# Kernel tuning notes

Hardware: AMD Instinct MI355X
Metric: run time of the kernel (lower is better)

## Reference

```python
import jax, jax.numpy as jnp
import numpy as np

B, T, C, H = 4, 2048, 1024, 16
D = C // H


def setup_inputs() -> dict:
    key = jax.random.key(0)
    ks = jax.random.split(key, 5)
    s = 0.02
    return {
        "x": jax.random.normal(ks[0], (B, T, C), dtype=jnp.float32),
        "W_attn": jax.random.normal(ks[1], (C, 3 * C), dtype=jnp.float32) * s,
        "b_attn": jax.random.normal(ks[2], (3 * C,), dtype=jnp.float32) * s,
        "W_proj": jax.random.normal(ks[3], (C, C), dtype=jnp.float32) * s,
        "b_proj": jax.random.normal(ks[4], (C,), dtype=jnp.float32) * s,
    }


def reference(x, W_attn, b_attn, W_proj, b_proj):
    # QKV projection: [B,T,3C]
    qkv = x @ W_attn + b_attn
    q, k, v = jnp.split(qkv, 3, axis=-1)
    # [B,T,C] -> [B,H,T,D]
    def to_heads(t):
        return t.reshape(B, T, H, D).transpose(0, 2, 1, 3)
    q, k, v = to_heads(q), to_heads(k), to_heads(v)
    scale = 1.0 / np.sqrt(D).astype(np.float32)
    # full (non-causal) attention scores [B,H,T,T]
    att = jnp.einsum("bhqd,bhkd->bhqk", q, k) * scale
    att = jax.nn.softmax(att, axis=-1)
    y = jnp.einsum("bhqk,bhkd->bhqd", att, v)
    y = y.transpose(0, 2, 1, 3).reshape(B, T, C)
    return y @ W_proj + b_proj
```

## Files before the change

### kernel.cpp

```cpp
#include <hip/hip_runtime.h>

#define BATCH 4
#define SEQ   2048
#define CDIM  1024
#define NHEAD 16
#define HDIM  64
#define BH    (BATCH * NHEAD)
#define MROWS (BATCH * SEQ)

typedef __attribute__((ext_vector_type(8))) short  short8;
typedef __attribute__((ext_vector_type(4))) float  floatx4;

#define MFMA_BF16(a, b, c) __builtin_amdgcn_mfma_f32_16x16x32_bf16((a), (b), (c), 0, 0, 0)

#define GLOAD16(g, l) __builtin_amdgcn_global_load_lds( \
    (__attribute__((address_space(1))) void*)(g),       \
    (__attribute__((address_space(3))) void*)(l), 16, 0, 0)

__device__ __forceinline__ unsigned short f2bf(float f) {
    union { float f; unsigned u; } v; v.f = f;
    unsigned u = v.u;
    return (unsigned short)((u + 0x7FFFu + ((u >> 16) & 1u)) >> 16);
}

__device__ __forceinline__ float fast_exp2(float x) {
#if __has_builtin(__builtin_amdgcn_exp2f)
    return __builtin_amdgcn_exp2f(x);
#else
    return exp2f(x);
#endif
}

__device__ __forceinline__ unsigned pack_bf16_trunc(float a, float b) {
    union { float f; unsigned u; } ua, ub;
    ua.f = a; ub.f = b;
    return __builtin_amdgcn_perm(ub.u, ua.u, 0x07060302u);
}

__global__ __launch_bounds__(256) void conv_bf16_kernel(
    const float* __restrict__ in, unsigned short* __restrict__ out)
{
    int i = (blockIdx.x * 256 + threadIdx.x) * 4;
    float4 v = *(const float4*)(in + i);
    ushort4 o;
    o.x = f2bf(v.x); o.y = f2bf(v.y); o.z = f2bf(v.z); o.w = f2bf(v.w);
    *(ushort4*)(out + i) = o;
}

__global__ __launch_bounds__(256) void conv_wt_kernel(
    const float* __restrict__ in, unsigned short* __restrict__ out, int K, int N)
{
    __shared__ float T[64][68];
    const int k0 = blockIdx.y * 64, n0 = blockIdx.x * 64;
    const int tid = threadIdx.x;
    const int r = tid >> 4, c4 = (tid & 15) * 4;
    #pragma unroll
    for (int i = 0; i < 4; ++i) {
        int row = r + i * 16;
        float4 v = *(const float4*)(in + (size_t)(k0 + row) * N + n0 + c4);
        T[row][c4 + 0] = v.x; T[row][c4 + 1] = v.y;
        T[row][c4 + 2] = v.z; T[row][c4 + 3] = v.w;
    }
    __syncthreads();
    #pragma unroll
    for (int i = 0; i < 4; ++i) {
        int nrow = r + i * 16;
        ushort4 o;
        o.x = f2bf(T[c4 + 0][nrow]); o.y = f2bf(T[c4 + 1][nrow]);
        o.z = f2bf(T[c4 + 2][nrow]); o.w = f2bf(T[c4 + 3][nrow]);
        *(ushort4*)(out + (size_t)(n0 + nrow) * K + k0 + c4) = o;
    }
}

__global__ __launch_bounds__(512, 2) void qkv_mfma_kernel(
    const unsigned short* __restrict__ A,
    const unsigned short* __restrict__ Bt,
    const float* __restrict__ bias,
    unsigned short* __restrict__ Qo,
    unsigned short* __restrict__ Ko,
    unsigned short* __restrict__ Vo)
{
    __shared__ __align__(16) unsigned short L[2 * 32768];

    const int tid = threadIdx.x;
    const int m0 = blockIdx.y * 256, n0 = blockIdx.x * 256;
    const int w = tid >> 6, lane = tid & 63;
    const int wr = w >> 2, wc = w & 3;
    const int lm = lane & 15, kg = lane >> 4;
    const int sw = lm & 7;

    floatx4 acc[2][4][2][2];
    const floatx4 zf = {0.f, 0.f, 0.f, 0.f};
    #pragma unroll
    for (int a = 0; a < 2; ++a)
        #pragma unroll
        for (int b = 0; b < 4; ++b)
            #pragma unroll
            for (int c = 0; c < 2; ++c)
                #pragma unroll
                for (int d = 0; d < 2; ++d) acc[a][b][c][d] = zf;

    short8 af[4][2], bf[2][2];

#define QSTAGE_A(B_, H_, KT_) do {                                            \
    unsigned short* _l = (unsigned short*)L + (B_) * 32768 + (H_) * 8192;     \
    _Pragma("unroll")                                                         \
    for (int _i = 0; _i < 2; ++_i) {                                          \
        int _s = _i * 512 + tid, _r = _s >> 3, _c = _s & 7;                   \
        GLOAD16(A + (size_t)(m0 + (H_) * 128 + _r) * CDIM + (KT_) * 64        \
                   + ((_c ^ (_r & 7)) * 8), _l + _s * 8);                     \
    } } while (0)

#define QSTAGE_B(B_, H_, KT_) do {                                            \
    unsigned short* _l = (unsigned short*)L + (B_) * 32768 + 16384 + (H_) * 8192; \
    _Pragma("unroll")                                                         \
    for (int _i = 0; _i < 2; ++_i) {                                          \
        int _s = _i * 512 + tid, _r = _s >> 3, _c = _s & 7;                   \
        GLOAD16(Bt + (size_t)(n0 + (H_) * 128 + _r) * CDIM + (KT_) * 64       \
                   + ((_c ^ (_r & 7)) * 8), _l + _s * 8);                     \
    } } while (0)

#define QLOAD_A(B_, H_) do {                                                  \
    const unsigned short* _p = (const unsigned short*)L + (B_) * 32768 + (H_) * 8192; \
    _Pragma("unroll")                                                         \
    for (int _m = 0; _m < 4; ++_m) {                                          \
        int _row = wr * 64 + _m * 16 + lm;                                    \
        _Pragma("unroll")                                                     \
        for (int _k = 0; _k < 2; ++_k)                                        \
            af[_m][_k] = *(const short8*)(_p + _row * 64                      \
                          + (((_k * 4 + kg) ^ sw) * 8));                      \
    } } while (0)

#define QLOAD_B(B_, H_) do {                                                  \
    const unsigned short* _p = (const unsigned short*)L + (B_) * 32768 + 16384 + (H_) * 8192; \
    _Pragma("unroll")                                                         \
    for (int _n = 0; _n < 2; ++_n) {                                          \
        int _row = wc * 32 + _n * 16 + lm;                                    \
        _Pragma("unroll")                                                     \
        for (int _k = 0; _k < 2; ++_k)                                        \
            bf[_n][_k] = *(const short8*)(_p + _row * 64                      \
                          + (((_k * 4 + kg) ^ sw) * 8));                      \
    } } while (0)

#define QMFMA(HH_, HP_) do {                                                  \
    _Pragma("unroll") for (int _k = 0; _k < 2; ++_k)                          \
    _Pragma("unroll") for (int _m = 0; _m < 4; ++_m)                          \
    _Pragma("unroll") for (int _n = 0; _n < 2; ++_n)                          \
        acc[HH_][_m][HP_][_n] =                                               \
            MFMA_BF16(af[_m][_k], bf[_n][_k], acc[HH_][_m][HP_][_n]);         \
    } while (0)

#define QPHASE(HH_, HP_, LA_, LB_, STAGE_, VM_) do {                          \
    if (LA_) QLOAD_A(buf, HH_);                                               \
    if (LB_) QLOAD_B(buf, HP_);                                               \
    STAGE_;                                                                   \
    asm volatile("s_waitcnt vmcnt(" #VM_ ")" ::: "memory");                   \
    __builtin_amdgcn_s_barrier();                                             \
    asm volatile("s_waitcnt lgkmcnt(0)" ::: "memory");                        \
    __builtin_amdgcn_sched_barrier(0);                                        \
    __builtin_amdgcn_s_setprio(1);                                            \
    QMFMA(HH_, HP_);                                                          \
    __builtin_amdgcn_s_setprio(0);                                            \
    __builtin_amdgcn_s_barrier();                                             \
    __builtin_amdgcn_sched_barrier(0);                                        \
    } while (0)

    QSTAGE_A(0, 0, 0); QSTAGE_B(0, 0, 0); QSTAGE_B(0, 1, 0); QSTAGE_A(0, 1, 0);
    asm volatile("s_waitcnt vmcnt(4)" ::: "memory");
    __builtin_amdgcn_s_barrier();

    #pragma unroll 1
    for (int t = 0; t < CDIM / 64 - 1; ++t) {
        const int buf = t & 1, nb = buf ^ 1;
        QPHASE(0, 0, 1, 1, QSTAGE_A(nb, 0, t + 1), 4);
        QPHASE(0, 1, 0, 1, QSTAGE_B(nb, 0, t + 1), 4);
        QPHASE(1, 1, 1, 0, QSTAGE_B(nb, 1, t + 1), 4);
        QPHASE(1, 0, 0, 1, QSTAGE_A(nb, 1, t + 1), 4);
    }
    {
        const int buf = (CDIM / 64 - 1) & 1;
        QPHASE(0, 0, 1, 1, ((void)0), 2);
        QPHASE(0, 1, 0, 1, ((void)0), 0);
        QPHASE(1, 1, 1, 0, ((void)0), 0);
        QPHASE(1, 0, 0, 1, ((void)0), 0);
    }

#undef QPHASE
#undef QMFMA
#undef QLOAD_B
#undef QLOAD_A
#undef QSTAGE_B
#undef QSTAGE_A

    #pragma unroll
    for (int hp = 0; hp < 2; ++hp) {
        #pragma unroll
        for (int nt = 0; nt < 2; ++nt) {
            int col = n0 + hp * 128 + wc * 32 + nt * 16 + lm;
            float bv = bias[col];
            int which = col >> 10;
            int c1 = col & 1023;
            int h = c1 >> 6, d = c1 & 63;
            #pragma unroll
            for (int hh = 0; hh < 2; ++hh) {
                #pragma unroll
                for (int mt = 0; mt < 4; ++mt) {
                    int m = m0 + hh * 128 + wr * 64 + mt * 16 + kg * 4;
                    int b = m >> 11;
                    int tt = m & 2047;
                    int bh = b * NHEAD + h;
                    floatx4 a = acc[hh][mt][hp][nt];
                    if (which == 2) {
                        ushort4 o;
                        o.x = f2bf(a[0] + bv);
                        o.y = f2bf(a[1] + bv);
                        o.z = f2bf(a[2] + bv);
                        o.w = f2bf(a[3] + bv);
                        *(ushort4*)(Vo + ((size_t)bh * 64 + d) * SEQ + tt) = o;
                    } else {
                        unsigned short* dst = (which == 0) ? Qo : Ko;
                        float qs = (which == 0) ? 0.18033688011112042f : 1.0f;
                        #pragma unroll
                        for (int r = 0; r < 4; ++r)
                            dst[((size_t)bh * SEQ + tt + r) * 64 + d] =
                                f2bf((a[r] + bv) * qs);
                    }
                }
            }
        }
    }
}

#define GBUF (128 * 32)

__device__ __forceinline__ void gemm_stage(
    const unsigned short* __restrict__ A, const unsigned short* __restrict__ Bt,
    int K, int m0, int n0, int k0, unsigned short* As, unsigned short* Bs, int tid)
{
    #pragma unroll
    for (int i = 0; i < 2; ++i) {
        int ci = i * 256 + tid;
        GLOAD16(A  + (size_t)(m0 + (ci >> 2)) * K + k0 + (ci & 3) * 8, As + ci * 8);
        GLOAD16(Bt + (size_t)(n0 + (ci >> 2)) * K + k0 + (ci & 3) * 8, Bs + ci * 8);
    }
}

__global__ __launch_bounds__(256) void proj_mfma_kernel(
    const unsigned short* __restrict__ A,
    const unsigned short* __restrict__ Bt,
    const float* __restrict__ bias,
    float* __restrict__ out)
{
    const int K = CDIM;
    __shared__ __align__(16) unsigned short As2[2 * GBUF];
    __shared__ __align__(16) unsigned short Bs2[2 * GBUF];

    const int tid = threadIdx.x;
    const int m0 = blockIdx.y * 128, n0 = blockIdx.x * 128;
    const int w = tid >> 6, lane = tid & 63;
    const int wm = (w >> 1) * 64, wn = (w & 1) * 64;
    const int lm = lane & 15, kg = lane >> 4;

    floatx4 acc[4][4];
    const floatx4 zf = {0.f, 0.f, 0.f, 0.f};
    #pragma unroll
    for (int mt = 0; mt < 4; ++mt)
        #pragma unroll
        for (int nt = 0; nt < 4; ++nt) acc[mt][nt] = zf;

    gemm_stage(A, Bt, K, m0, n0, 0, As2, Bs2, tid);

    #pragma unroll 1
    for (int kt = 0; kt < K / 32; ++kt) {
        __syncthreads();
        if (kt + 1 < K / 32)
            gemm_stage(A, Bt, K, m0, n0, (kt + 1) * 32,
                       As2 + ((kt + 1) & 1) * GBUF, Bs2 + ((kt + 1) & 1) * GBUF, tid);
        const unsigned short* As = As2 + (kt & 1) * GBUF;
        const unsigned short* Bs = Bs2 + (kt & 1) * GBUF;
        short8 af[4], bfr[4];
        #pragma unroll
        for (int t = 0; t < 4; ++t) {
            af[t]  = *(const short8*)(As + (wm + t * 16 + lm) * 32 + kg * 8);
            bfr[t] = *(const short8*)(Bs + (wn + t * 16 + lm) * 32 + kg * 8);
        }
        #pragma unroll
        for (int mt = 0; mt < 4; ++mt)
            #pragma unroll
            for (int nt = 0; nt < 4; ++nt)
                acc[mt][nt] = MFMA_BF16(af[mt], bfr[nt], acc[mt][nt]);
    }

    #pragma unroll
    for (int nt = 0; nt < 4; ++nt) {
        int col = n0 + wn + nt * 16 + lm;
        float bv = bias[col];
        #pragma unroll
        for (int mt = 0; mt < 4; ++mt) {
            int mbase = m0 + wm + mt * 16 + kg * 4;
            #pragma unroll
            for (int r = 0; r < 4; ++r)
                out[(size_t)(mbase + r) * CDIM + col] = acc[mt][nt][r] + bv;
        }
    }
}

#define BUFSH 8192

__device__ __forceinline__ void attn_stage_tile(
    const unsigned short* __restrict__ Kg,
    const unsigned short* __restrict__ Vg,
    size_t base, int kb, unsigned short* buf, int tid)
{
    unsigned short* Kb_ = buf;
    unsigned short* Vb_ = buf + 4096;
    #pragma unroll
    for (int i = 0; i < 2; ++i) {
        int lin = i * 256 + tid;
        int srow = lin >> 3;
        int chunk = lin & 7;
        int s2 = srow & 31;
        int grow = (srow & 32) + ((s2 >> 2) & 3) * 8 + ((s2 >> 4) & 1) * 4 + (s2 & 3);
        int gch = chunk ^ (srow & 7);
        GLOAD16(Kg + base + (size_t)(kb * 64 + grow) * 64 + gch * 8, Kb_ + lin * 8);
        GLOAD16(Vg + base + (size_t)srow * SEQ + kb * 64 + gch * 8, Vb_ + lin * 8);
    }
}

__global__ __launch_bounds__(256) void attn_mfma_kernel(
    const unsigned short* __restrict__ Qg,
    const unsigned short* __restrict__ Kg,
    const unsigned short* __restrict__ Vg,
    unsigned short* __restrict__ Y)
{
    __shared__ __align__(16) unsigned short Smem[2 * BUFSH];

    const int tid = threadIdx.x, w = tid >> 6, lane = tid & 63;
    const int lm = lane & 15, kg = lane >> 4;
    const int qb = blockIdx.x, bh = blockIdx.y;
    const size_t base = (size_t)bh * SEQ * 64;

    short8 qf[2][2];
    #pragma unroll
    for (int nt = 0; nt < 2; ++nt)
        #pragma unroll
        for (int c = 0; c < 2; ++c)
            qf[nt][c] = *(const short8*)(
                Qg + base + (size_t)(qb * 128 + w * 32 + nt * 16 + lm) * 64 + c * 32 + kg * 8);

    const floatx4 zf = {0.f, 0.f, 0.f, 0.f};
    floatx4 O[2][4];
    #pragma unroll
    for (int nt = 0; nt < 2; ++nt)
        #pragma unroll
        for (int nd = 0; nd < 4; ++nd) O[nt][nd] = zf;
    float lsum[2] = {0.f, 0.f};

    attn_stage_tile(Kg, Vg, base, 0, Smem, tid);

    #pragma unroll 1
    for (int kb = 0; kb < SEQ / 64; ++kb) {
        __syncthreads();
        if (kb + 1 < SEQ / 64)
            attn_stage_tile(Kg, Vg, base, kb + 1, Smem + ((kb + 1) & 1) * BUFSH, tid);

        const unsigned short* Ksb = Smem + (kb & 1) * BUFSH;
        const unsigned short* Vsb = Ksb + 4096;
        const int sw = (lm & 7);

        #pragma unroll
        for (int ch = 0; ch < 2; ++ch) {
            uint4 pa[2];
            #pragma unroll
            for (int mt = 0; mt < 2; ++mt) {
                floatx4 st[2];
                #pragma unroll
                for (int nt = 0; nt < 2; ++nt) st[nt] = zf;
                #pragma unroll
                for (int c = 0; c < 2; ++c) {
                    short8 kf = *(const short8*)(
                        Ksb + (ch * 32 + mt * 16 + lm) * 64 + ((c * 4 + kg) ^ sw) * 8);
                    #pragma unroll
                    for (int nt = 0; nt < 2; ++nt)
                        st[nt] = MFMA_BF16(kf, qf[nt][c], st[nt]);
                }
                #pragma unroll
                for (int nt = 0; nt < 2; ++nt) {
                    float e0 = fast_exp2(st[nt][0]);
                    float e1 = fast_exp2(st[nt][1]);
                    float e2 = fast_exp2(st[nt][2]);
                    float e3 = fast_exp2(st[nt][3]);
                    lsum[nt] += (e0 + e1) + (e2 + e3);
                    if (mt == 0) {
                        pa[nt].x = pack_bf16_trunc(e0, e1);
                        pa[nt].y = pack_bf16_trunc(e2, e3);
                    } else {
                        pa[nt].z = pack_bf16_trunc(e0, e1);
                        pa[nt].w = pack_bf16_trunc(e2, e3);
                    }
                }
            }
            #pragma unroll
            for (int nd = 0; nd < 4; ++nd) {
                short8 vb = *(const short8*)(
                    Vsb + (nd * 16 + lm) * 64 + ((ch * 4 + kg) ^ sw) * 8);
                #pragma unroll
                for (int nt = 0; nt < 2; ++nt) {
                    short8 paf;
                    __builtin_memcpy(&paf, &pa[nt], 16);
                    O[nt][nd] = MFMA_BF16(paf, vb, O[nt][nd]);
                }
            }
        }
    }

    #pragma unroll
    for (int nt = 0; nt < 2; ++nt) {
        lsum[nt] += __shfl_xor(lsum[nt], 16);
        lsum[nt] += __shfl_xor(lsum[nt], 32);
    }
    float linv[2][4];
    #pragma unroll
    for (int mq = 0; mq < 2; ++mq)
        #pragma unroll
        for (int r = 0; r < 4; ++r)
            linv[mq][r] = 1.0f / __shfl(lsum[mq], kg * 4 + r);

    const int b = bh >> 4, h = bh & 15;
    #pragma unroll
    for (int mq = 0; mq < 2; ++mq)
        #pragma unroll
        for (int r = 0; r < 4; ++r) {
            int t = qb * 128 + w * 32 + mq * 16 + kg * 4 + r;
            #pragma unroll
            for (int nd = 0; nd < 4; ++nd)
                Y[((size_t)(b * SEQ + t)) * CDIM + h * 64 + nd * 16 + lm] =
                    f2bf(O[mq][nd][r] * linv[mq][r]);
        }
}

extern "C" void kernel_launch(void* const* d_in, const int* in_sizes, int n_in,
                              void* d_out, int out_size, void* d_ws, size_t ws_size,
                              hipStream_t stream) {
    const float* x      = (const float*)d_in[0];
    const float* W_attn = (const float*)d_in[1];
    const float* b_attn = (const float*)d_in[2];
    const float* W_proj = (const float*)d_in[3];
    const float* b_proj = (const float*)d_in[4];
    float* out = (float*)d_out;

    char* ws = (char*)d_ws;
    unsigned short* xb  = (unsigned short*)(ws);
    unsigned short* Wat = (unsigned short*)(ws + (size_t)16777216);
    unsigned short* Wpt = (unsigned short*)(ws + (size_t)23068672);
    unsigned short* Qb  = (unsigned short*)(ws + (size_t)25165824);
    unsigned short* Kb  = (unsigned short*)(ws + (size_t)41943040);
    unsigned short* Vtb = (unsigned short*)(ws + (size_t)58720256);
    unsigned short* Yb  = (unsigned short*)(ws + (size_t)75497472);

    conv_bf16_kernel<<<dim3(MROWS * CDIM / 1024), 256, 0, stream>>>(x, xb);
    conv_wt_kernel<<<dim3(3 * CDIM / 64, CDIM / 64), 256, 0, stream>>>(
        W_attn, Wat, CDIM, 3 * CDIM);
    conv_wt_kernel<<<dim3(CDIM / 64, CDIM / 64), 256, 0, stream>>>(
        W_proj, Wpt, CDIM, CDIM);

    qkv_mfma_kernel<<<dim3(3 * CDIM / 256, MROWS / 256), 512, 0, stream>>>(
        xb, Wat, b_attn, Qb, Kb, Vtb);

    attn_mfma_kernel<<<dim3(SEQ / 128, BH), 256, 0, stream>>>(Qb, Kb, Vtb, Yb);

    proj_mfma_kernel<<<dim3(CDIM / 128, MROWS / 128), 256, 0, stream>>>(
        Yb, Wpt, b_proj, out);
}
```

Baseline: 274.9 us.

## Merge conversion kernels into one launch and swizzle QKV GEMM block order

The three fp32-to-bf16 conversion kernels (activations, transposed attention weight, transposed projection weight) become one kernel that dispatches on block index. This removes two launches and lets the small weight transposes overlap with the activation conversion. The QKV GEMM grid is flattened and remapped so that blocks dispatched in sequence share the same weight column tile across different row tiles, which should improve L2 or XCD-local cache reuse. The trade-off is that all blocks of the merged kernel reserve the transpose tile's shared memory, which may lower occupancy for the activation-conversion blocks.

```diff
diff --git a/kernel.cpp b/kernel.cpp
--- a/kernel.cpp
+++ b/kernel.cpp
@@ -37,22 +37,32 @@
     return __builtin_amdgcn_perm(ub.u, ua.u, 0x07060302u);
 }
 
-__global__ __launch_bounds__(256) void conv_bf16_kernel(
-    const float* __restrict__ in, unsigned short* __restrict__ out)
-{
-    int i = (blockIdx.x * 256 + threadIdx.x) * 4;
-    float4 v = *(const float4*)(in + i);
-    ushort4 o;
-    o.x = f2bf(v.x); o.y = f2bf(v.y); o.z = f2bf(v.z); o.w = f2bf(v.w);
-    *(ushort4*)(out + i) = o;
-}
-
-__global__ __launch_bounds__(256) void conv_wt_kernel(
-    const float* __restrict__ in, unsigned short* __restrict__ out, int K, int N)
-{
+__global__ __launch_bounds__(256) void conv_all_kernel(
+    const float* __restrict__ x,  unsigned short* __restrict__ xb,
+    const float* __restrict__ Wa, unsigned short* __restrict__ Wat,
+    const float* __restrict__ Wp, unsigned short* __restrict__ Wpt)
+{
+    const int bx = blockIdx.x, tid = threadIdx.x;
+    if (bx < 8192) {
+        int i = (bx * 256 + tid) * 4;
+        float4 v = *(const float4*)(x + i);
+        ushort4 o;
+        o.x = f2bf(v.x); o.y = f2bf(v.y); o.z = f2bf(v.z); o.w = f2bf(v.w);
+        *(ushort4*)(xb + i) = o;
+        return;
+    }
     __shared__ float T[64][68];
-    const int k0 = blockIdx.y * 64, n0 = blockIdx.x * 64;
-    const int tid = threadIdx.x;
+    const float* in; unsigned short* out; int N, k0, n0;
+    if (bx < 8192 + 768) {
+        int t = bx - 8192;
+        in = Wa; out = Wat; N = 3 * CDIM;
+        n0 = (t % 48) * 64; k0 = (t / 48) * 64;
+    } else {
+        int t = bx - 8960;
+        in = Wp; out = Wpt; N = CDIM;
+        n0 = (t & 15) * 64; k0 = (t >> 4) * 64;
+    }
+    const int K = CDIM;
     const int r = tid >> 4, c4 = (tid & 15) * 4;
     #pragma unroll
     for (int i = 0; i < 4; ++i) {
@@ -83,7 +93,9 @@
     __shared__ __align__(16) unsigned short L[2 * 32768];
 
     const int tid = threadIdx.x;
-    const int m0 = blockIdx.y * 256, n0 = blockIdx.x * 256;
+    const int flat = blockIdx.x;
+    const int swz = (flat & 7) * 48 + (flat >> 3);
+    const int m0 = (swz / 12) * 256, n0 = (swz % 12) * 256;
     const int w = tid >> 6, lane = tid & 63;
     const int wr = w >> 2, wc = w & 3;
     const int lm = lane & 15, kg = lane >> 4;
@@ -458,13 +470,10 @@
     unsigned short* Vtb = (unsigned short*)(ws + (size_t)58720256);
     unsigned short* Yb  = (unsigned short*)(ws + (size_t)75497472);
 
-    conv_bf16_kernel<<<dim3(MROWS * CDIM / 1024), 256, 0, stream>>>(x, xb);
-    conv_wt_kernel<<<dim3(3 * CDIM / 64, CDIM / 64), 256, 0, stream>>>(
-        W_attn, Wat, CDIM, 3 * CDIM);
-    conv_wt_kernel<<<dim3(CDIM / 64, CDIM / 64), 256, 0, stream>>>(
-        W_proj, Wpt, CDIM, CDIM);
-
-    qkv_mfma_kernel<<<dim3(3 * CDIM / 256, MROWS / 256), 512, 0, stream>>>(
+    conv_all_kernel<<<dim3(9216), 256, 0, stream>>>(
+        x, xb, W_attn, Wat, W_proj, Wpt);
+
+    qkv_mfma_kernel<<<dim3(384), 512, 0, stream>>>(
         xb, Wat, b_attn, Qb, Kb, Vtb);
 
     attn_mfma_kernel<<<dim3(SEQ / 128, BH), 256, 0, stream>>>(Qb, Kb, Vtb, Yb);
```

Measured after the change: 269.4 us, median of 2. -2.0%, faster.
